# Performance work log

Measured on AMD Instinct MI355X. Metric: run time of the kernel, lower is better.

## Reference

```python
import jax, jax.numpy as jnp
import numpy as np

NUM_HEADS = 16
VALUE_SIZE = 64
MODEL_SIZE = 1024
BATCH = 4
SEQ = 1024


def setup_inputs() -> dict:
    key = jax.random.key(0)
    ks = jax.random.split(key, 5)
    scale = 1.0 / np.sqrt(MODEL_SIZE)
    x = jax.random.normal(ks[0], (BATCH, SEQ, MODEL_SIZE), dtype=jnp.float32)
    w_q = jax.random.normal(ks[1], (MODEL_SIZE, NUM_HEADS * VALUE_SIZE), dtype=jnp.float32) * scale
    w_kv = jax.random.normal(ks[2], (MODEL_SIZE, NUM_HEADS * VALUE_SIZE), dtype=jnp.float32) * scale
    w_o = jax.random.normal(ks[3], (NUM_HEADS * VALUE_SIZE, MODEL_SIZE), dtype=jnp.float32) * scale
    # original init is Constant(0.0); use small random values for a non-trivial test
    k_weights = jax.random.normal(ks[4], (1, NUM_HEADS, 1, VALUE_SIZE), dtype=jnp.float32) * 0.02
    return {"x": x, "w_q": w_q, "w_kv": w_kv, "w_o": w_o, "k_weights": k_weights}


def reference(x, w_q, w_kv, w_o, k_weights):
    b, L, d = x.shape
    h, v = NUM_HEADS, VALUE_SIZE
    # projections (no bias); q scaled by 1/sqrt(model_size)
    q = (x @ w_q) * (1.0 / jnp.sqrt(jnp.asarray(d, x.dtype)))
    q = q.reshape(b, L, h, v).transpose(0, 2, 1, 3)    # b h l v
    kv = (x @ w_kv).reshape(b, L, h, v).transpose(0, 2, 1, 3)  # b h l v
    # learned per-head key scaling on the shared k=v tensor
    k = kv * (1.0 + k_weights)
    logits = jnp.einsum('bhik,bhjk->bhij', q, k)       # b h L L
    mask = jnp.tril(jnp.ones((L, L), dtype=bool))
    logits = jnp.where(mask, logits, jnp.asarray(-1e6, logits.dtype))
    a = jax.nn.softmax(logits, axis=-1)
    y = jnp.einsum('bhij,bhjv->bhiv', a, kv)           # attend over shared kv
    y = y.transpose(0, 2, 1, 3).reshape(b, L, h * v)
    return y @ w_o
```

## Files before the change

### kernel.cpp

```cpp
#include <hip/hip_runtime.h>
#include <hip/hip_bf16.h>
#include <stdint.h>

#define BATCH 4
#define SEQ   1024
#define DMODEL 1024
#define NH    16
#define DV    64

typedef short bf8 __attribute__((ext_vector_type(8)));
typedef float f4  __attribute__((ext_vector_type(4)));

static __device__ __forceinline__ short f2bf(float f) {
    union { float f; uint32_t u; } a; a.f = f;
    uint32_t r = a.u + 0x7FFF + ((a.u >> 16) & 1);
    return (short)(r >> 16);
}

static __device__ __forceinline__ f4 mfma16(bf8 a, bf8 b, f4 c) {
    return __builtin_amdgcn_mfma_f32_16x16x32_bf16(a, b, c, 0, 0, 0);
}

static __device__ __forceinline__ void gload16(const short* g, short* l) {
    __builtin_amdgcn_global_load_lds((const __attribute__((address_space(1))) void*)g,
                                     (__attribute__((address_space(3))) void*)l,
                                     16, 0, 0);
}


__global__ void prep_kernel(const float* __restrict__ x,
                            const float* __restrict__ wq, const float* __restrict__ wkv,
                            const float* __restrict__ wo,
                            short* __restrict__ xb,
                            short* __restrict__ wqkvt, short* __restrict__ wot) {
    int z = blockIdx.z;
    int tx = threadIdx.x, ty = threadIdx.y;
    if (z >= 3) {
        int i = (((z - 3) * 1024 + blockIdx.y * 32 + blockIdx.x) << 8) + ty * 32 + tx;
        float4 v = ((const float4*)x)[i];
        short4 o;
        o.x = f2bf(v.x); o.y = f2bf(v.y); o.z = f2bf(v.z); o.w = f2bf(v.w);
        ((short4*)xb)[i] = o;
        return;
    }
    __shared__ float tile[32][33];
    const float* w = (z == 0) ? wq : (z == 1) ? wkv : wo;
    short* wt = (z == 0) ? wqkvt : (z == 1) ? (wqkvt + (1u << 20)) : wot;
    int bx = blockIdx.x, by = blockIdx.y;
    #pragma unroll
    for (int i = 0; i < 4; i++)
        tile[ty + i * 8][tx] = w[(size_t)(by * 32 + ty + i * 8) * 1024 + bx * 32 + tx];
    __syncthreads();
    #pragma unroll
    for (int i = 0; i < 4; i++)
        wt[(size_t)(bx * 32 + ty + i * 8) * 1024 + by * 32 + tx] = f2bf(tile[tx][ty + i * 8]);
}


__global__ __launch_bounds__(256) void gemm_proj_kernel(
    const short* __restrict__ A, const short* __restrict__ Bt,
    const float* __restrict__ kw,
    short* __restrict__ q_out, short* __restrict__ kv_out, short* __restrict__ kvT_out)
{
    __shared__ short SM[32768];
    const int K = DMODEL;

    int tid = threadIdx.x;
    int wave = tid >> 6, lane = tid & 63;
    int quad = lane >> 4, l16 = lane & 15;

    int flat = blockIdx.x + (blockIdx.y << 4);
    int xcd = flat & 7, pos = flat >> 3;
    int nby = ((xcd >> 1) << 3) + (pos >> 3);
    int nbx = ((xcd & 1) << 3) + (pos & 7);
    int m0 = nby * 128;
    int n0 = nbx * 128;

    int wm = (wave >> 1) * 64;
    int wn = (wave & 1) * 64;
    int sw = l16 & 7;

    f4 acc[4][4] = {};

    auto stage = [&](int buf, int k0) {
        short* As = SM + buf * 16384;
        short* Bs = As + 8192;
        #pragma unroll
        for (int c = 0; c < 4; c++) {
            int flt = c * 256 + tid;
            int row = flt >> 3;
            int seg = (flt & 7) ^ (row & 7);
            gload16(A + (size_t)(m0 + row) * K + k0 + seg * 8, As + flt * 8);
        }
        #pragma unroll
        for (int c = 0; c < 4; c++) {
            int flt = c * 256 + tid;
            int row = flt >> 3;
            int seg = (flt & 7) ^ (row & 7);
            gload16(Bt + (size_t)(n0 + row) * K + k0 + seg * 8, Bs + flt * 8);
        }
    };

    stage(0, 0);
    for (int k0 = 0; k0 < K; k0 += 64) {
        int buf = (k0 >> 6) & 1;
        __syncthreads();
        if (k0 + 64 < K) stage(buf ^ 1, k0 + 64);
        const short* As = SM + buf * 16384;
        const short* Bs = As + 8192;
        #pragma unroll
        for (int kk = 0; kk < 2; kk++) {
            bf8 ar[4], br[4];
            #pragma unroll
            for (int i = 0; i < 4; i++)
                ar[i] = *(const bf8*)(As + (wm + i * 16 + l16) * 64 + ((kk * 4 + quad) ^ sw) * 8);
            #pragma unroll
            for (int j = 0; j < 4; j++)
                br[j] = *(const bf8*)(Bs + (wn + j * 16 + l16) * 64 + ((kk * 4 + quad) ^ sw) * 8);
            #pragma unroll
            for (int i = 0; i < 4; i++) {
                #pragma unroll
                for (int j = 0; j < 4; j++)
                    acc[i][j] = mfma16(ar[i], br[j], acc[i][j]);
            }
        }
    }

    if (n0 < 1024) {
        #pragma unroll
        for (int j = 0; j < 4; j++) {
            int n = n0 + wn + j * 16 + l16;
            float kws = 0.03125f * (1.0f + kw[n]);
            #pragma unroll
            for (int i = 0; i < 4; i++) {
                int mb = m0 + wm + i * 16 + quad * 4;
                q_out[(size_t)(mb + 0) * 1024 + n] = f2bf(acc[i][j][0] * kws);
                q_out[(size_t)(mb + 1) * 1024 + n] = f2bf(acc[i][j][1] * kws);
                q_out[(size_t)(mb + 2) * 1024 + n] = f2bf(acc[i][j][2] * kws);
                q_out[(size_t)(mb + 3) * 1024 + n] = f2bf(acc[i][j][3] * kws);
            }
        }
        return;
    }

    #pragma unroll
    for (int j = 0; j < 4; j++) {
        int n2 = n0 - 1024 + wn + j * 16 + l16;
        #pragma unroll
        for (int i = 0; i < 4; i++) {
            int mb = m0 + wm + i * 16 + quad * 4;
            kv_out[(size_t)(mb + 0) * 1024 + n2] = f2bf(acc[i][j][0]);
            kv_out[(size_t)(mb + 1) * 1024 + n2] = f2bf(acc[i][j][1]);
            kv_out[(size_t)(mb + 2) * 1024 + n2] = f2bf(acc[i][j][2]);
            kv_out[(size_t)(mb + 3) * 1024 + n2] = f2bf(acc[i][j][3]);
        }
    }

    {
        const int TST = 136;
        short* T = SM;
        __syncthreads();
        short* Tw = T + (wave & 1) * (64 * TST);
        #pragma unroll
        for (int j = 0; j < 4; j++) {
            int nl = j * 16 + l16;
            #pragma unroll
            for (int i = 0; i < 4; i++) {
                short4 tv;
                tv.x = f2bf(acc[i][j][0]); tv.y = f2bf(acc[i][j][1]);
                tv.z = f2bf(acc[i][j][2]); tv.w = f2bf(acc[i][j][3]);
                *(short4*)(Tw + nl * TST + wm + i * 16 + quad * 4) = tv;
            }
        }
        __syncthreads();
        int n2base = n0 - 1024;
        int mloc = m0 & 1023;
        int bq = m0 >> 10;
        #pragma unroll
        for (int c = 0; c < 8; c++) {
            int flt = c * 256 + tid;
            int row = flt >> 4;
            int seg = flt & 15;
            bf8 vseg = *(const bf8*)(T + (row >> 6) * (64 * TST) + (row & 63) * TST + seg * 8);
            int n2 = n2base + row;
            int bh = (bq << 4) + (n2 >> 6);
            *(bf8*)(kvT_out + (size_t)(bh * 64 + (n2 & 63)) * 1024 + mloc + seg * 8) = vseg;
        }
    }
}


__global__ __launch_bounds__(256) void gemm_out_kernel(
    const short* __restrict__ A, const short* __restrict__ Bt,
    float* __restrict__ c_out)
{
    __shared__ short SM[32768];
    const int K = DMODEL;

    int tid = threadIdx.x;
    int wave = tid >> 6, lane = tid & 63;
    int quad = lane >> 4, l16 = lane & 15;

    int flat = blockIdx.x + (blockIdx.y << 3);
    int xcd = flat & 7, pos = flat >> 3;
    int nby = ((xcd >> 1) << 3) + (pos >> 2);
    int nbx = ((xcd & 1) << 2) + (pos & 3);
    int m0 = nby * 128;
    int n0 = nbx * 128;

    int wm = (wave >> 1) * 64;
    int wn = (wave & 1) * 64;
    int sw = l16 & 7;

    f4 acc[4][4] = {};

    auto stage = [&](int buf, int k0) {
        short* As = SM + buf * 16384;
        short* Bs = As + 8192;
        #pragma unroll
        for (int c = 0; c < 4; c++) {
            int flt = c * 256 + tid;
            int row = flt >> 3;
            int seg = (flt & 7) ^ (row & 7);
            gload16(A + (size_t)(m0 + row) * K + k0 + seg * 8, As + flt * 8);
        }
        #pragma unroll
        for (int c = 0; c < 4; c++) {
            int flt = c * 256 + tid;
            int row = flt >> 3;
            int seg = (flt & 7) ^ (row & 7);
            gload16(Bt + (size_t)(n0 + row) * K + k0 + seg * 8, Bs + flt * 8);
        }
    };

    stage(0, 0);
    for (int k0 = 0; k0 < K; k0 += 64) {
        int buf = (k0 >> 6) & 1;
        __syncthreads();
        if (k0 + 64 < K) stage(buf ^ 1, k0 + 64);
        const short* As = SM + buf * 16384;
        const short* Bs = As + 8192;
        #pragma unroll
        for (int kk = 0; kk < 2; kk++) {
            bf8 ar[4], br[4];
            #pragma unroll
            for (int i = 0; i < 4; i++)
                ar[i] = *(const bf8*)(As + (wm + i * 16 + l16) * 64 + ((kk * 4 + quad) ^ sw) * 8);
            #pragma unroll
            for (int j = 0; j < 4; j++)
                br[j] = *(const bf8*)(Bs + (wn + j * 16 + l16) * 64 + ((kk * 4 + quad) ^ sw) * 8);
            #pragma unroll
            for (int i = 0; i < 4; i++) {
                #pragma unroll
                for (int j = 0; j < 4; j++)
                    acc[i][j] = mfma16(ar[i], br[j], acc[i][j]);
            }
        }
    }

    #pragma unroll
    for (int j = 0; j < 4; j++) {
        int n = n0 + wn + j * 16 + l16;
        #pragma unroll
        for (int i = 0; i < 4; i++) {
            int mb = m0 + wm + i * 16 + quad * 4;
            c_out[(size_t)(mb + 0) * 1024 + n] = acc[i][j][0];
            c_out[(size_t)(mb + 1) * 1024 + n] = acc[i][j][1];
            c_out[(size_t)(mb + 2) * 1024 + n] = acc[i][j][2];
            c_out[(size_t)(mb + 3) * 1024 + n] = acc[i][j][3];
        }
    }
}


#define PLD 72

__global__ __launch_bounds__(256) void attn_kernel(
    const short* __restrict__ qg, const short* __restrict__ kvg,
    const short* __restrict__ kvTg, short* __restrict__ yg)
{
    int w = blockIdx.x + (blockIdx.y << 3);
    int bh = ((w >> 6) << 3) + (w & 7);
    int x = (w >> 3) & 7;
    int b = bh >> 4, h = bh & 15;
    int tid = threadIdx.x;
    int wave = tid >> 6, lane = tid & 63;
    int quad = lane >> 4, l16 = lane & 15;
    int qa0 = x * 64;
    int qb0 = (15 - x) * 64;
    int ntiles = 16 - x;

    __shared__ short Ks[2][64 * 64];
    __shared__ short Vs[2][64 * 64];
    __shared__ short Ps[4][2 * 16 * PLD];
    short* myPB = &Ps[wave][0];
    short* myPA = &Ps[wave][16 * PLD];

    const short* qpa = qg + (size_t)(b * 1024 + qa0 + wave * 16 + l16) * 1024 + h * 64;
    const short* qpb = qg + (size_t)(b * 1024 + qb0 + wave * 16 + l16) * 1024 + h * 64;
    bf8 qa_0 = *(const bf8*)(qpa + quad * 8);
    bf8 qa_1 = *(const bf8*)(qpa + 32 + quad * 8);
    bf8 qb_0 = *(const bf8*)(qpb + quad * 8);
    bf8 qb_1 = *(const bf8*)(qpb + 32 + quad * 8);

    bf8 ones;
    #pragma unroll
    for (int j = 0; j < 8; j++) ones[j] = (short)0x3F80;

    f4 oa[4] = {}, ob[4] = {};
    f4 lsa = {}, lsb = {};
    int rowbaseA = qa0 + wave * 16 + quad * 4;
    int rowbaseB = qb0 + wave * 16 + quad * 4;

    auto stage = [&](int jt) {
        short* dstK = &Ks[jt & 1][0];
        short* dstV = &Vs[jt & 1][0];
        int j0 = jt * 64;
        #pragma unroll
        for (int k = 0; k < 2; k++) {
            int flat = k * 256 + tid;
            int row = flat >> 3;
            int lseg = (flat & 7) ^ (row & 7);
            gload16(kvg + (size_t)(b * 1024 + j0 + row) * 1024 + h * 64 + lseg * 8,
                    dstK + flat * 8);
            gload16(kvTg + (size_t)(bh * 64 + row) * 1024 + j0 + lseg * 8,
                    dstV + flat * 8);
        }
    };

    auto qk = [&](bf8 qf0, bf8 qf1, const short* K, f4 (&s)[4]) {
        __builtin_amdgcn_s_setprio(1);
        #pragma unroll
        for (int c = 0; c < 4; c++) {
            int row = c * 16 + l16;
            int swz = row & 7;
            bf8 kb0 = *(const bf8*)(K + row * 64 + (quad ^ swz) * 8);
            bf8 kb1 = *(const bf8*)(K + row * 64 + (((quad + 4) ^ swz)) * 8);
            f4 t = {};
            t = mfma16(qf0, kb0, t);
            t = mfma16(qf1, kb1, t);
            s[c] = t;
        }
        __builtin_amdgcn_s_setprio(0);
    };

    auto expstoreU = [&](f4 (&s)[4], short* P) {
        #pragma unroll
        for (int r = 0; r < 4; r++) {
            int prow = quad * 4 + r;
            P[prow * PLD + l16]      = f2bf(__expf(s[0][r]));
            P[prow * PLD + 16 + l16] = f2bf(__expf(s[1][r]));
            P[prow * PLD + 32 + l16] = f2bf(__expf(s[2][r]));
            P[prow * PLD + 48 + l16] = f2bf(__expf(s[3][r]));
        }
    };

    auto expstoreM = [&](f4 (&s)[4], int rowbase, int j0, short* P) {
        #pragma unroll
        for (int r = 0; r < 4; r++) {
            int qi = rowbase + r;
            float p0 = (j0 + l16      <= qi) ? __expf(s[0][r]) : 0.0f;
            float p1 = (j0 + 16 + l16 <= qi) ? __expf(s[1][r]) : 0.0f;
            float p2 = (j0 + 32 + l16 <= qi) ? __expf(s[2][r]) : 0.0f;
            float p3 = (j0 + 48 + l16 <= qi) ? __expf(s[3][r]) : 0.0f;
            int prow = quad * 4 + r;
            P[prow * PLD + l16]      = f2bf(p0);
            P[prow * PLD + 16 + l16] = f2bf(p1);
            P[prow * PLD + 32 + l16] = f2bf(p2);
            P[prow * PLD + 48 + l16] = f2bf(p3);
        }
    };

    auto pv = [&](const short* P, const short* V, f4 (&o)[4], f4& lsum) {
        bf8 pf0 = *(const bf8*)(P + l16 * PLD + quad * 8);
        bf8 pf1 = *(const bf8*)(P + l16 * PLD + 32 + quad * 8);
        __builtin_amdgcn_s_setprio(1);
        lsum = mfma16(pf0, ones, lsum);
        lsum = mfma16(pf1, ones, lsum);
        #pragma unroll
        for (int t = 0; t < 4; t++) {
            int vrow = t * 16 + l16;
            int swz = vrow & 7;
            bf8 vb0 = *(const bf8*)(V + vrow * 64 + (quad ^ swz) * 8);
            bf8 vb1 = *(const bf8*)(V + vrow * 64 + (((quad + 4) ^ swz)) * 8);
            o[t] = mfma16(pf0, vb0, o[t]);
            o[t] = mfma16(pf1, vb1, o[t]);
        }
        __builtin_amdgcn_s_setprio(0);
    };

    stage(0);

    for (int jt = 0; jt < ntiles; jt++) {
        __syncthreads();
        if (jt + 1 < ntiles) stage(jt + 1);
        const short* K = &Ks[jt & 1][0];
        const short* V = &Vs[jt & 1][0];
        int j0 = jt * 64;
        bool doA = (jt <= x);

        if (doA) {
            f4 sb[4], sa[4];
            __builtin_amdgcn_s_setprio(1);
            #pragma unroll
            for (int c = 0; c < 4; c++) {
                int row = c * 16 + l16;
                int swz = row & 7;
                bf8 kb0 = *(const bf8*)(K + row * 64 + (quad ^ swz) * 8);
                bf8 kb1 = *(const bf8*)(K + row * 64 + (((quad + 4) ^ swz)) * 8);
                f4 tb = {};
                tb = mfma16(qb_0, kb0, tb);
                tb = mfma16(qb_1, kb1, tb);
                sb[c] = tb;
                f4 ta = {};
                ta = mfma16(qa_0, kb0, ta);
                ta = mfma16(qa_1, kb1, ta);
                sa[c] = ta;
            }
            __builtin_amdgcn_s_setprio(0);
            expstoreU(sb, myPB);
            if (jt == x) expstoreM(sa, rowbaseA, j0, myPA);
            else         expstoreU(sa, myPA);
            bf8 pb0 = *(const bf8*)(myPB + l16 * PLD + quad * 8);
            bf8 pb1 = *(const bf8*)(myPB + l16 * PLD + 32 + quad * 8);
            bf8 pa0 = *(const bf8*)(myPA + l16 * PLD + quad * 8);
            bf8 pa1 = *(const bf8*)(myPA + l16 * PLD + 32 + quad * 8);
            __builtin_amdgcn_s_setprio(1);
            lsb = mfma16(pb0, ones, lsb);
            lsb = mfma16(pb1, ones, lsb);
            lsa = mfma16(pa0, ones, lsa);
            lsa = mfma16(pa1, ones, lsa);
            #pragma unroll
            for (int t = 0; t < 4; t++) {
                int vrow = t * 16 + l16;
                int swz = vrow & 7;
                bf8 vb0 = *(const bf8*)(V + vrow * 64 + (quad ^ swz) * 8);
                bf8 vb1 = *(const bf8*)(V + vrow * 64 + (((quad + 4) ^ swz)) * 8);
                ob[t] = mfma16(pb0, vb0, ob[t]);
                ob[t] = mfma16(pb1, vb1, ob[t]);
                oa[t] = mfma16(pa0, vb0, oa[t]);
                oa[t] = mfma16(pa1, vb1, oa[t]);
            }
            __builtin_amdgcn_s_setprio(0);
        } else {
            f4 sb[4];
            qk(qb_0, qb_1, K, sb);
            if (jt == ntiles - 1) expstoreM(sb, rowbaseB, j0, myPB);
            else                  expstoreU(sb, myPB);
            pv(myPB, V, ob, lsb);
        }
    }

    {
        float r0 = 1.0f / lsa[0], r1 = 1.0f / lsa[1], r2 = 1.0f / lsa[2], r3 = 1.0f / lsa[3];
        #pragma unroll
        for (int t = 0; t < 4; t++) {
            size_t base = (size_t)(b * SEQ + rowbaseA) * (NH * DV) + h * DV + t * 16 + l16;
            yg[base]                 = f2bf(oa[t][0] * r0);
            yg[base + 1 * (NH * DV)] = f2bf(oa[t][1] * r1);
            yg[base + 2 * (NH * DV)] = f2bf(oa[t][2] * r2);
            yg[base + 3 * (NH * DV)] = f2bf(oa[t][3] * r3);
        }
    }
    {
        float r0 = 1.0f / lsb[0], r1 = 1.0f / lsb[1], r2 = 1.0f / lsb[2], r3 = 1.0f / lsb[3];
        #pragma unroll
        for (int t = 0; t < 4; t++) {
            size_t base = (size_t)(b * SEQ + rowbaseB) * (NH * DV) + h * DV + t * 16 + l16;
            yg[base]                 = f2bf(ob[t][0] * r0);
            yg[base + 1 * (NH * DV)] = f2bf(ob[t][1] * r1);
            yg[base + 2 * (NH * DV)] = f2bf(ob[t][2] * r2);
            yg[base + 3 * (NH * DV)] = f2bf(ob[t][3] * r3);
        }
    }
}


extern "C" void kernel_launch(void* const* d_in, const int* in_sizes, int n_in,
                              void* d_out, int out_size, void* d_ws, size_t ws_size,
                              hipStream_t stream) {
    const float* x    = (const float*)d_in[0];
    const float* w_q  = (const float*)d_in[1];
    const float* w_kv = (const float*)d_in[2];
    const float* w_o  = (const float*)d_in[3];
    const float* kw   = (const float*)d_in[4];
    float* out = (float*)d_out;

    char* ws = (char*)d_ws;
    short* xb    = (short*)(ws);
    short* wqkvt = (short*)(ws + ( 8u << 20));
    short* wot   = (short*)(ws + (12u << 20));
    short* qp    = (short*)(ws + (14u << 20));
    short* kvb   = (short*)(ws + (22u << 20));
    short* kvT   = (short*)(ws + (30u << 20));
    short* yb    = (short*)(ws + (38u << 20));

    prep_kernel<<<dim3(32, 32, 7), dim3(32, 8), 0, stream>>>(
        x, w_q, w_kv, w_o, xb, wqkvt, wot);

    gemm_proj_kernel<<<dim3(16, 32), 256, 0, stream>>>(
        xb, wqkvt, kw, qp, kvb, kvT);

    attn_kernel<<<dim3(8, BATCH * NH), 256, 0, stream>>>(qp, kvb, kvT, yb);

    gemm_out_kernel<<<dim3(8, 32), 256, 0, stream>>>(yb, wot, out);
}
```

Baseline: 144.3 us.

## Fuse x fp32-to-bf16 conversion into projection GEMM A-tile loading

Drops the separate pass that converted x to bf16 in the prep kernel. The projection GEMM now reads fp32 x straight into registers, converts it to bf16 and writes it to LDS after the MFMA loop, so the next tile's load overlaps compute. This avoids writing and re-reading the 8 MB bf16 copy of x. In exchange the A loads now go through registers, with more VGPR pressure and twice the global bytes per A tile, and x is re-read by all 16 column blocks.

```diff
diff --git a/kernel.cpp b/kernel.cpp
--- a/kernel.cpp
+++ b/kernel.cpp
@@ -28,21 +28,11 @@
 }
 
 
-__global__ void prep_kernel(const float* __restrict__ x,
-                            const float* __restrict__ wq, const float* __restrict__ wkv,
+__global__ void prep_kernel(const float* __restrict__ wq, const float* __restrict__ wkv,
                             const float* __restrict__ wo,
-                            short* __restrict__ xb,
                             short* __restrict__ wqkvt, short* __restrict__ wot) {
     int z = blockIdx.z;
     int tx = threadIdx.x, ty = threadIdx.y;
-    if (z >= 3) {
-        int i = (((z - 3) * 1024 + blockIdx.y * 32 + blockIdx.x) << 8) + ty * 32 + tx;
-        float4 v = ((const float4*)x)[i];
-        short4 o;
-        o.x = f2bf(v.x); o.y = f2bf(v.y); o.z = f2bf(v.z); o.w = f2bf(v.w);
-        ((short4*)xb)[i] = o;
-        return;
-    }
     __shared__ float tile[32][33];
     const float* w = (z == 0) ? wq : (z == 1) ? wkv : wo;
     short* wt = (z == 0) ? wqkvt : (z == 1) ? (wqkvt + (1u << 20)) : wot;
@@ -58,7 +48,7 @@
 
 
 __global__ __launch_bounds__(256) void gemm_proj_kernel(
-    const short* __restrict__ A, const short* __restrict__ Bt,
+    const float* __restrict__ X, const short* __restrict__ Bt,
     const float* __restrict__ kw,
     short* __restrict__ q_out, short* __restrict__ kv_out, short* __restrict__ kvT_out)
 {
@@ -81,17 +71,34 @@
     int sw = l16 & 7;
 
     f4 acc[4][4] = {};
-
-    auto stage = [&](int buf, int k0) {
-        short* As = SM + buf * 16384;
-        short* Bs = As + 8192;
+    float4 areg[4][2];
+
+    auto aload = [&](int k0) {
         #pragma unroll
         for (int c = 0; c < 4; c++) {
             int flt = c * 256 + tid;
             int row = flt >> 3;
             int seg = (flt & 7) ^ (row & 7);
-            gload16(A + (size_t)(m0 + row) * K + k0 + seg * 8, As + flt * 8);
-        }
+            const float* src = X + (size_t)(m0 + row) * K + k0 + seg * 8;
+            areg[c][0] = *(const float4*)(src);
+            areg[c][1] = *(const float4*)(src + 4);
+        }
+    };
+    auto awrite = [&](int buf) {
+        short* As = SM + buf * 16384;
+        #pragma unroll
+        for (int c = 0; c < 4; c++) {
+            int flt = c * 256 + tid;
+            bf8 v;
+            v[0] = f2bf(areg[c][0].x); v[1] = f2bf(areg[c][0].y);
+            v[2] = f2bf(areg[c][0].z); v[3] = f2bf(areg[c][0].w);
+            v[4] = f2bf(areg[c][1].x); v[5] = f2bf(areg[c][1].y);
+            v[6] = f2bf(areg[c][1].z); v[7] = f2bf(areg[c][1].w);
+            *(bf8*)(As + flt * 8) = v;
+        }
+    };
+    auto stageB = [&](int buf, int k0) {
+        short* Bs = SM + buf * 16384 + 8192;
         #pragma unroll
         for (int c = 0; c < 4; c++) {
             int flt = c * 256 + tid;
@@ -101,11 +108,15 @@
         }
     };
 
-    stage(0, 0);
+    aload(0);
+    stageB(0, 0);
+    awrite(0);
+
     for (int k0 = 0; k0 < K; k0 += 64) {
         int buf = (k0 >> 6) & 1;
         __syncthreads();
-        if (k0 + 64 < K) stage(buf ^ 1, k0 + 64);
+        bool more = (k0 + 64 < K);
+        if (more) { aload(k0 + 64); stageB(buf ^ 1, k0 + 64); }
         const short* As = SM + buf * 16384;
         const short* Bs = As + 8192;
         #pragma unroll
@@ -124,6 +135,7 @@
                     acc[i][j] = mfma16(ar[i], br[j], acc[i][j]);
             }
         }
+        if (more) awrite(buf ^ 1);
     }
 
     if (n0 < 1024) {
@@ -487,7 +499,6 @@
     float* out = (float*)d_out;
 
     char* ws = (char*)d_ws;
-    short* xb    = (short*)(ws);
     short* wqkvt = (short*)(ws + ( 8u << 20));
     short* wot   = (short*)(ws + (12u << 20));
     short* qp    = (short*)(ws + (14u << 20));
@@ -495,11 +506,11 @@
     short* kvT   = (short*)(ws + (30u << 20));
     short* yb    = (short*)(ws + (38u << 20));
 
-    prep_kernel<<<dim3(32, 32, 7), dim3(32, 8), 0, stream>>>(
-        x, w_q, w_kv, w_o, xb, wqkvt, wot);
+    prep_kernel<<<dim3(32, 32, 3), dim3(32, 8), 0, stream>>>(
+        w_q, w_kv, w_o, wqkvt, wot);
 
     gemm_proj_kernel<<<dim3(16, 32), 256, 0, stream>>>(
-        xb, wqkvt, kw, qp, kvb, kvT);
+        x, wqkvt, kw, qp, kvb, kvT);
 
     attn_kernel<<<dim3(8, BATCH * NH), 256, 0, stream>>>(qp, kvb, kvT, yb);
 
```

New measurement: 149.2 us. 1.03x slower.
